# Kernel tuning notes

Hardware: AMD Instinct MI355X
Metric: run time of the kernel (lower is better)

## Reference

```python
import jax, jax.numpy as jnp
import numpy as np

B, T, D, U = 32, 4096, 256, 256


def setup_inputs() -> dict:
    key = jax.random.key(0)
    ks = jax.random.split(key, 5)
    s = 1.0 / np.sqrt(D)
    return {
        "query": jax.random.normal(ks[0], (B, D), jnp.float32),
        "values": jax.random.normal(ks[1], (B, T, D), jnp.float32),
        "W1": jax.random.normal(ks[2], (D, U), jnp.float32) * s,
        "b1": jnp.zeros((U,), jnp.float32),
        "W2": jax.random.normal(ks[3], (D, U), jnp.float32) * s,
        "b2": jnp.zeros((U,), jnp.float32),
        "V": jax.random.normal(ks[4], (U, 1), jnp.float32) * (1.0 / np.sqrt(U)),
        "bV": jnp.zeros((1,), jnp.float32),
    }


def reference(query, values, W1, b1, W2, b2, V, bV):
    # score[b,t,u] = tanh(values @ W1 + b1 + (query @ W2 + b2)[:,None,:])
    proj_v = jnp.einsum("btd,du->btu", values, W1) + b1        # [B,T,U]
    proj_q = (query @ W2 + b2)[:, None, :]                      # [B,1,U]
    score = jnp.tanh(proj_v + proj_q) @ V + bV                  # [B,T,1]
    attn = jax.nn.softmax(score, axis=1)                        # softmax over T
    context = jnp.sum(attn * values, axis=1)                    # [B,D]
    return (context, attn)
```

## Files before the change

### kernel.cpp

```cpp
#include <hip/hip_runtime.h>
#include <hip/hip_bf16.h>

typedef __attribute__((ext_vector_type(4))) float f32x4;
typedef __attribute__((ext_vector_type(8))) short s16x8;
typedef __attribute__((ext_vector_type(4))) short s16x4;

static constexpr int Bn = 32;
static constexpr int Tn = 4096;
static constexpr int Dn = 256;
static constexpr int Un = 256;
static constexpr int CH = Tn / 64;

__device__ __forceinline__ ushort f2bf(float f) {
    unsigned x = __float_as_uint(f);
    x += 0x7fffu + ((x >> 16) & 1u);
    return (ushort)(x >> 16);
}
__device__ __forceinline__ float bf2f(ushort u) {
    return __uint_as_float(((unsigned)u) << 16);
}

__device__ __forceinline__ float fast_tanh(float x) {
    float ax = fabsf(x);
    float e = __expf(-2.0f * ax);
    float r = __fdividef(1.0f - e, 1.0f + e);
    return copysignf(r, x);
}

__global__ __launch_bounds__(256) void k_prep(const float* __restrict__ W1,
                                              ushort* __restrict__ W1T,
                                              const float* __restrict__ query,
                                              const float* __restrict__ W2,
                                              const float* __restrict__ b1,
                                              const float* __restrict__ b2,
                                              float* __restrict__ qb) {
    __shared__ float qs[Dn];
    if (blockIdx.x < 256) {
        const int u = blockIdx.x, d = threadIdx.x;
        W1T[u * Dn + d] = f2bf(W1[d * Un + u]);
    } else {
        const int b = blockIdx.x - 256, u = threadIdx.x;
        qs[u] = query[b * Dn + u];
        __syncthreads();
        float acc = b1[u] + b2[u];
        #pragma unroll 8
        for (int d = 0; d < Dn; ++d) acc += qs[d] * W2[d * Un + u];
        qb[b * Un + u] = acc;
    }
}

__global__ __launch_bounds__(256, 4) void k_fused(const float* __restrict__ values,
                                                  const ushort* __restrict__ W1T,
                                                  const float* __restrict__ qb,
                                                  const float* __restrict__ Vw,
                                                  const float* __restrict__ bV,
                                                  float* __restrict__ scores,
                                                  float* __restrict__ pm,
                                                  float* __restrict__ ps,
                                                  float* __restrict__ pctx) {
    __shared__ __align__(16) ushort Al[64][264];
    __shared__ float sred[4][64];
    __shared__ float slp[64];
    __shared__ f32x4 red[4][64];
    const int tid = threadIdx.x;
    const int b = blockIdx.y;
    const int c = blockIdx.x;
    const int t0 = c * 64;
    const int wid = tid >> 6;
    const int lane = tid & 63;
    const int l15 = lane & 15;
    const int hi = lane >> 4;

    const float* vbase = values + ((size_t)b * Tn + t0) * Dn;
    #pragma unroll
    for (int i = 0; i < 8; ++i) {
        int flat = i * 2048 + tid * 8;
        int row = flat >> 8, col = flat & 255;
        const float4 f0 = *(const float4*)&vbase[row * Dn + col];
        const float4 f1 = *(const float4*)&vbase[row * Dn + col + 4];
        s16x8 p;
        p[0] = (short)f2bf(f0.x); p[1] = (short)f2bf(f0.y);
        p[2] = (short)f2bf(f0.z); p[3] = (short)f2bf(f0.w);
        p[4] = (short)f2bf(f1.x); p[5] = (short)f2bf(f1.y);
        p[6] = (short)f2bf(f1.z); p[7] = (short)f2bf(f1.w);
        *(s16x8*)&Al[row][col] = p;
    }

    const ushort* wbase = W1T + (size_t)(wid * 64 + l15) * Dn + hi * 8;

    f32x4 acc[4][4];
    #pragma unroll
    for (int tt = 0; tt < 4; ++tt)
        #pragma unroll
        for (int ut = 0; ut < 4; ++ut) acc[tt][ut] = (f32x4){0.f, 0.f, 0.f, 0.f};

    s16x8 bfn0[4], bfn1[4];
    #pragma unroll
    for (int ut = 0; ut < 4; ++ut)
        bfn0[ut] = *(const s16x8*)&wbase[(size_t)ut * 16 * Dn];
    #pragma unroll
    for (int ut = 0; ut < 4; ++ut)
        bfn1[ut] = *(const s16x8*)&wbase[(size_t)ut * 16 * Dn + 32];

    __syncthreads();

    #pragma unroll
    for (int kc = 0; kc < 8; ++kc) {
        s16x8 bf[4];
        #pragma unroll
        for (int ut = 0; ut < 4; ++ut) { bf[ut] = bfn0[ut]; bfn0[ut] = bfn1[ut]; }
        if (kc < 6) {
            #pragma unroll
            for (int ut = 0; ut < 4; ++ut)
                bfn1[ut] = *(const s16x8*)&wbase[(size_t)ut * 16 * Dn + (kc + 2) * 32];
        }
        const int k0 = kc * 32;
        s16x8 af[4];
        #pragma unroll
        for (int tt = 0; tt < 4; ++tt)
            af[tt] = *(const s16x8*)&Al[tt * 16 + l15][k0 + hi * 8];
        #pragma unroll
        for (int tt = 0; tt < 4; ++tt)
            #pragma unroll
            for (int ut = 0; ut < 4; ++ut)
                acc[tt][ut] = __builtin_amdgcn_mfma_f32_16x16x32_bf16(af[tt], bf[ut], acc[tt][ut], 0, 0, 0);
    }

    float Vreg[4], qreg[4];
    #pragma unroll
    for (int ut = 0; ut < 4; ++ut) {
        int u = wid * 64 + ut * 16 + l15;
        Vreg[ut] = Vw[u];
        qreg[ut] = qb[b * Un + u];
    }

    float psc[4][4];
    #pragma unroll
    for (int tt = 0; tt < 4; ++tt)
        #pragma unroll
        for (int i = 0; i < 4; ++i) psc[tt][i] = 0.f;
    #pragma unroll
    for (int tt = 0; tt < 4; ++tt)
        #pragma unroll
        for (int ut = 0; ut < 4; ++ut)
            #pragma unroll
            for (int i = 0; i < 4; ++i)
                psc[tt][i] += fast_tanh(acc[tt][ut][i] + qreg[ut]) * Vreg[ut];

    #pragma unroll
    for (int tt = 0; tt < 4; ++tt)
        #pragma unroll
        for (int i = 0; i < 4; ++i) {
            float v = psc[tt][i];
            v += __shfl_xor(v, 1, 64);
            v += __shfl_xor(v, 2, 64);
            v += __shfl_xor(v, 4, 64);
            v += __shfl_xor(v, 8, 64);
            if (l15 == 0) sred[wid][tt * 16 + hi * 4 + i] = v;
        }
    __syncthreads();

    if (tid < 64) {
        float s = sred[0][tid] + sred[1][tid] + sred[2][tid] + sred[3][tid] + bV[0];
        scores[b * Tn + t0 + tid] = s;
        float m = s;
        #pragma unroll
        for (int off = 32; off > 0; off >>= 1) m = fmaxf(m, __shfl_xor(m, off, 64));
        float p = __expf(s - m);
        float S = p;
        #pragma unroll
        for (int off = 32; off > 0; off >>= 1) S += __shfl_xor(S, off, 64);
        slp[tid] = p;
        if (tid == 0) { pm[b * CH + c] = m; ps[b * CH + c] = S; }
    }
    __syncthreads();

    const int d4 = (tid & 63) * 4, tg = tid >> 6;
    f32x4 a = (f32x4){0.f, 0.f, 0.f, 0.f};
    #pragma unroll 4
    for (int t = tg; t < 64; t += 4) {
        const float p = slp[t];
        const s16x4 v = *(const s16x4*)&Al[t][d4];
        a[0] += p * bf2f((ushort)v[0]);
        a[1] += p * bf2f((ushort)v[1]);
        a[2] += p * bf2f((ushort)v[2]);
        a[3] += p * bf2f((ushort)v[3]);
    }
    red[tg][tid & 63] = a;
    __syncthreads();
    if (tg == 0) {
        const f32x4 r0 = red[0][tid], r1 = red[1][tid], r2 = red[2][tid], r3 = red[3][tid];
        f32x4 o = r0 + r1 + r2 + r3;
        *(f32x4*)&pctx[((size_t)b * CH + c) * Dn + d4] = o;
    }
}

__global__ __launch_bounds__(256) void k_reduce(const float* __restrict__ pm,
                                                const float* __restrict__ ps,
                                                const float* __restrict__ pctx,
                                                float* __restrict__ context,
                                                float* __restrict__ MS) {
    const int b = blockIdx.x, d = threadIdx.x;
    float M = -1e30f;
    #pragma unroll 8
    for (int c = 0; c < CH; ++c) M = fmaxf(M, pm[b * CH + c]);
    float S = 0.f, ctx = 0.f;
    #pragma unroll 4
    for (int c = 0; c < CH; ++c) {
        const float w = __expf(pm[b * CH + c] - M);
        S += w * ps[b * CH + c];
        ctx += w * pctx[((size_t)b * CH + c) * Dn + d];
    }
    context[b * Dn + d] = __fdividef(ctx, S);
    if (d == 0) { MS[b * 2] = M; MS[b * 2 + 1] = S; }
}

__global__ __launch_bounds__(256) void k_attn(float* __restrict__ attn,
                                              const float* __restrict__ MS) {
    const int b = blockIdx.y;
    const int base = b * Tn + blockIdx.x * 1024 + threadIdx.x * 4;
    const float M = MS[b * 2];
    const float invS = __fdividef(1.0f, MS[b * 2 + 1]);
    float4 s = *(const float4*)&attn[base];
    s.x = __expf(s.x - M) * invS;
    s.y = __expf(s.y - M) * invS;
    s.z = __expf(s.z - M) * invS;
    s.w = __expf(s.w - M) * invS;
    *(float4*)&attn[base] = s;
}

extern "C" void kernel_launch(void* const* d_in, const int* in_sizes, int n_in,
                              void* d_out, int out_size, void* d_ws, size_t ws_size,
                              hipStream_t stream) {
    const float* query  = (const float*)d_in[0];
    const float* values = (const float*)d_in[1];
    const float* W1     = (const float*)d_in[2];
    const float* b1     = (const float*)d_in[3];
    const float* W2     = (const float*)d_in[4];
    const float* b2     = (const float*)d_in[5];
    const float* Vw     = (const float*)d_in[6];
    const float* bV     = (const float*)d_in[7];

    float* context = (float*)d_out;
    float* attn    = (float*)d_out + Bn * Dn;

    float*  pctx = (float*)d_ws;
    float*  pm   = pctx + (size_t)Bn * CH * Dn;
    float*  ps   = pm + Bn * CH;
    float*  qb   = ps + Bn * CH;
    float*  MS   = qb + Bn * Un;
    ushort* W1T  = (ushort*)(MS + Bn * 2);

    k_prep<<<dim3(256 + Bn), dim3(256), 0, stream>>>(W1, W1T, query, W2, b1, b2, qb);
    k_fused<<<dim3(CH, Bn), dim3(256), 0, stream>>>(values, W1T, qb, Vw, bV,
                                                    attn, pm, ps, pctx);
    k_reduce<<<dim3(Bn), dim3(256), 0, stream>>>(pm, ps, pctx, context, MS);
    k_attn<<<dim3(Tn / 1024, Bn), dim3(256), 0, stream>>>(attn, MS);
}
```

Measured before the change: 78.46 us.

## Make fused kernel persistent over 256 rows with register-staged prefetch and online softmax

Each block now loops over eight 32-row chunks of values (256 rows per block, 16 blocks per batch) instead of handling one 64-row tile. The next chunk's fp32 values are prefetched into registers while the current chunk is converted to bf16 in a double-buffered LDS tile and run through the MFMA projection. The softmax max, sum and context are accumulated online across chunks, which shrinks the partial buffers and the work in k_reduce. The cost is that W1T fragments are reloaded from global memory for every chunk, there are more barriers per chunk, and the grid drops to 512 blocks with a launch bound of 2 waves, which lowers parallelism.

```diff
diff --git a/kernel.cpp b/kernel.cpp
--- a/kernel.cpp
+++ b/kernel.cpp
@@ -9,7 +9,7 @@
 static constexpr int Tn = 4096;
 static constexpr int Dn = 256;
 static constexpr int Un = 256;
-static constexpr int CH = Tn / 64;
+static constexpr int NBLK = 16;
 
 __device__ __forceinline__ ushort f2bf(float f) {
     unsigned x = __float_as_uint(f);
@@ -49,82 +49,30 @@
     }
 }
 
-__global__ __launch_bounds__(256, 4) void k_fused(const float* __restrict__ values,
+__global__ __launch_bounds__(256, 2) void k_fused(const float* __restrict__ values,
                                                   const ushort* __restrict__ W1T,
                                                   const float* __restrict__ qb,
                                                   const float* __restrict__ Vw,
                                                   const float* __restrict__ bV,
                                                   float* __restrict__ scores,
-                                                  float* __restrict__ pm,
-                                                  float* __restrict__ ps,
+                                                  float* __restrict__ pM,
+                                                  float* __restrict__ pS,
                                                   float* __restrict__ pctx) {
-    __shared__ __align__(16) ushort Al[64][264];
-    __shared__ float sred[4][64];
-    __shared__ float slp[64];
-    __shared__ f32x4 red[4][64];
+    __shared__ __align__(16) ushort Bl[2][32][264];
+    __shared__ float sred[4][32];
+    __shared__ float slp[32];
+    __shared__ float sfac[2];
+    __shared__ float runMS[2];
+    __shared__ f32x4 cred[4][64];
+
     const int tid = threadIdx.x;
-    const int b = blockIdx.y;
-    const int c = blockIdx.x;
-    const int t0 = c * 64;
-    const int wid = tid >> 6;
-    const int lane = tid & 63;
-    const int l15 = lane & 15;
-    const int hi = lane >> 4;
-
-    const float* vbase = values + ((size_t)b * Tn + t0) * Dn;
-    #pragma unroll
-    for (int i = 0; i < 8; ++i) {
-        int flat = i * 2048 + tid * 8;
-        int row = flat >> 8, col = flat & 255;
-        const float4 f0 = *(const float4*)&vbase[row * Dn + col];
-        const float4 f1 = *(const float4*)&vbase[row * Dn + col + 4];
-        s16x8 p;
-        p[0] = (short)f2bf(f0.x); p[1] = (short)f2bf(f0.y);
-        p[2] = (short)f2bf(f0.z); p[3] = (short)f2bf(f0.w);
-        p[4] = (short)f2bf(f1.x); p[5] = (short)f2bf(f1.y);
-        p[6] = (short)f2bf(f1.z); p[7] = (short)f2bf(f1.w);
-        *(s16x8*)&Al[row][col] = p;
-    }
-
+    const int b = blockIdx.y, blk = blockIdx.x;
+    const int wid = tid >> 6, lane = tid & 63;
+    const int l15 = lane & 15, hi = lane >> 4;
+    const int d4 = (tid & 63) * 4, tg = tid >> 6;
+
+    const float* vbase = values + ((size_t)b * Tn + blk * 256) * Dn;
     const ushort* wbase = W1T + (size_t)(wid * 64 + l15) * Dn + hi * 8;
-
-    f32x4 acc[4][4];
-    #pragma unroll
-    for (int tt = 0; tt < 4; ++tt)
-        #pragma unroll
-        for (int ut = 0; ut < 4; ++ut) acc[tt][ut] = (f32x4){0.f, 0.f, 0.f, 0.f};
-
-    s16x8 bfn0[4], bfn1[4];
-    #pragma unroll
-    for (int ut = 0; ut < 4; ++ut)
-        bfn0[ut] = *(const s16x8*)&wbase[(size_t)ut * 16 * Dn];
-    #pragma unroll
-    for (int ut = 0; ut < 4; ++ut)
-        bfn1[ut] = *(const s16x8*)&wbase[(size_t)ut * 16 * Dn + 32];
-
-    __syncthreads();
-
-    #pragma unroll
-    for (int kc = 0; kc < 8; ++kc) {
-        s16x8 bf[4];
-        #pragma unroll
-        for (int ut = 0; ut < 4; ++ut) { bf[ut] = bfn0[ut]; bfn0[ut] = bfn1[ut]; }
-        if (kc < 6) {
-            #pragma unroll
-            for (int ut = 0; ut < 4; ++ut)
-                bfn1[ut] = *(const s16x8*)&wbase[(size_t)ut * 16 * Dn + (kc + 2) * 32];
-        }
-        const int k0 = kc * 32;
-        s16x8 af[4];
-        #pragma unroll
-        for (int tt = 0; tt < 4; ++tt)
-            af[tt] = *(const s16x8*)&Al[tt * 16 + l15][k0 + hi * 8];
-        #pragma unroll
-        for (int tt = 0; tt < 4; ++tt)
-            #pragma unroll
-            for (int ut = 0; ut < 4; ++ut)
-                acc[tt][ut] = __builtin_amdgcn_mfma_f32_16x16x32_bf16(af[tt], bf[ut], acc[tt][ut], 0, 0, 0);
-    }
 
     float Vreg[4], qreg[4];
     #pragma unroll
@@ -133,83 +81,167 @@
         Vreg[ut] = Vw[u];
         qreg[ut] = qb[b * Un + u];
     }
-
-    float psc[4][4];
-    #pragma unroll
-    for (int tt = 0; tt < 4; ++tt)
-        #pragma unroll
-        for (int i = 0; i < 4; ++i) psc[tt][i] = 0.f;
-    #pragma unroll
-    for (int tt = 0; tt < 4; ++tt)
+    const float bv = bV[0];
+
+    if (tid == 0) { runMS[0] = -1e30f; runMS[1] = 0.f; }
+
+    f32x4 stg[8];
+    #pragma unroll
+    for (int i = 0; i < 8; ++i) {
+        int idx = i * 256 + tid;
+        stg[i] = *(const f32x4*)&vbase[(idx >> 6) * Dn + (idx & 63) * 4];
+    }
+
+    f32x4 cacc = (f32x4){0.f, 0.f, 0.f, 0.f};
+
+    #pragma unroll 1
+    for (int ck = 0; ck < 8; ++ck) {
+        const int cur = ck & 1;
+
+        #pragma unroll
+        for (int i = 0; i < 8; ++i) {
+            int idx = i * 256 + tid;
+            s16x4 p;
+            p[0] = (short)f2bf(stg[i][0]); p[1] = (short)f2bf(stg[i][1]);
+            p[2] = (short)f2bf(stg[i][2]); p[3] = (short)f2bf(stg[i][3]);
+            *(s16x4*)&Bl[cur][idx >> 6][(idx & 63) * 4] = p;
+        }
+        __syncthreads();
+
+        if (ck < 7) {
+            const float* vb = vbase + (ck + 1) * 32 * Dn;
+            #pragma unroll
+            for (int i = 0; i < 8; ++i) {
+                int idx = i * 256 + tid;
+                stg[i] = *(const f32x4*)&vb[(idx >> 6) * Dn + (idx & 63) * 4];
+            }
+        }
+
+        s16x8 bfn0[4], bfn1[4];
         #pragma unroll
         for (int ut = 0; ut < 4; ++ut)
-            #pragma unroll
-            for (int i = 0; i < 4; ++i)
-                psc[tt][i] += fast_tanh(acc[tt][ut][i] + qreg[ut]) * Vreg[ut];
-
-    #pragma unroll
-    for (int tt = 0; tt < 4; ++tt)
-        #pragma unroll
-        for (int i = 0; i < 4; ++i) {
-            float v = psc[tt][i];
-            v += __shfl_xor(v, 1, 64);
-            v += __shfl_xor(v, 2, 64);
-            v += __shfl_xor(v, 4, 64);
-            v += __shfl_xor(v, 8, 64);
-            if (l15 == 0) sred[wid][tt * 16 + hi * 4 + i] = v;
-        }
-    __syncthreads();
-
-    if (tid < 64) {
-        float s = sred[0][tid] + sred[1][tid] + sred[2][tid] + sred[3][tid] + bV[0];
-        scores[b * Tn + t0 + tid] = s;
-        float m = s;
-        #pragma unroll
-        for (int off = 32; off > 0; off >>= 1) m = fmaxf(m, __shfl_xor(m, off, 64));
-        float p = __expf(s - m);
-        float S = p;
-        #pragma unroll
-        for (int off = 32; off > 0; off >>= 1) S += __shfl_xor(S, off, 64);
-        slp[tid] = p;
-        if (tid == 0) { pm[b * CH + c] = m; ps[b * CH + c] = S; }
-    }
-    __syncthreads();
-
-    const int d4 = (tid & 63) * 4, tg = tid >> 6;
-    f32x4 a = (f32x4){0.f, 0.f, 0.f, 0.f};
-    #pragma unroll 4
-    for (int t = tg; t < 64; t += 4) {
-        const float p = slp[t];
-        const s16x4 v = *(const s16x4*)&Al[t][d4];
-        a[0] += p * bf2f((ushort)v[0]);
-        a[1] += p * bf2f((ushort)v[1]);
-        a[2] += p * bf2f((ushort)v[2]);
-        a[3] += p * bf2f((ushort)v[3]);
-    }
-    red[tg][tid & 63] = a;
+            bfn0[ut] = *(const s16x8*)&wbase[(size_t)ut * 16 * Dn];
+        #pragma unroll
+        for (int ut = 0; ut < 4; ++ut)
+            bfn1[ut] = *(const s16x8*)&wbase[(size_t)ut * 16 * Dn + 32];
+
+        f32x4 acc[2][4];
+        #pragma unroll
+        for (int tt = 0; tt < 2; ++tt)
+            #pragma unroll
+            for (int ut = 0; ut < 4; ++ut) acc[tt][ut] = (f32x4){0.f, 0.f, 0.f, 0.f};
+
+        #pragma unroll
+        for (int kc = 0; kc < 8; ++kc) {
+            s16x8 bf[4];
+            #pragma unroll
+            for (int ut = 0; ut < 4; ++ut) { bf[ut] = bfn0[ut]; bfn0[ut] = bfn1[ut]; }
+            if (kc < 6) {
+                #pragma unroll
+                for (int ut = 0; ut < 4; ++ut)
+                    bfn1[ut] = *(const s16x8*)&wbase[(size_t)ut * 16 * Dn + (kc + 2) * 32];
+            }
+            s16x8 af[2];
+            #pragma unroll
+            for (int tt = 0; tt < 2; ++tt)
+                af[tt] = *(const s16x8*)&Bl[cur][tt * 16 + l15][kc * 32 + hi * 8];
+            #pragma unroll
+            for (int tt = 0; tt < 2; ++tt)
+                #pragma unroll
+                for (int ut = 0; ut < 4; ++ut)
+                    acc[tt][ut] = __builtin_amdgcn_mfma_f32_16x16x32_bf16(af[tt], bf[ut], acc[tt][ut], 0, 0, 0);
+        }
+
+        float psc[2][4];
+        #pragma unroll
+        for (int tt = 0; tt < 2; ++tt)
+            #pragma unroll
+            for (int i = 0; i < 4; ++i) psc[tt][i] = 0.f;
+        #pragma unroll
+        for (int tt = 0; tt < 2; ++tt)
+            #pragma unroll
+            for (int ut = 0; ut < 4; ++ut)
+                #pragma unroll
+                for (int i = 0; i < 4; ++i)
+                    psc[tt][i] += fast_tanh(acc[tt][ut][i] + qreg[ut]) * Vreg[ut];
+        #pragma unroll
+        for (int tt = 0; tt < 2; ++tt)
+            #pragma unroll
+            for (int i = 0; i < 4; ++i) {
+                float v = psc[tt][i];
+                v += __shfl_xor(v, 1, 64);
+                v += __shfl_xor(v, 2, 64);
+                v += __shfl_xor(v, 4, 64);
+                v += __shfl_xor(v, 8, 64);
+                if (l15 == 0) sred[wid][tt * 16 + hi * 4 + i] = v;
+            }
+        __syncthreads();
+
+        if (tid < 64) {
+            const int row = lane & 31;
+            float s = sred[0][row] + sred[1][row] + sred[2][row] + sred[3][row] + bv;
+            if (lane < 32) scores[b * Tn + blk * 256 + ck * 32 + row] = s;
+            float m = s;
+            #pragma unroll
+            for (int off = 16; off > 0; off >>= 1) m = fmaxf(m, __shfl_xor(m, off, 64));
+            float p = __expf(s - m);
+            float S = p;
+            #pragma unroll
+            for (int off = 16; off > 0; off >>= 1) S += __shfl_xor(S, off, 64);
+            if (lane < 32) slp[row] = p;
+            if (lane == 0) {
+                float Mold = runMS[0];
+                float Mnew = fmaxf(Mold, m);
+                float sco = __expf(Mold - Mnew);
+                float scc = __expf(m - Mnew);
+                sfac[0] = sco; sfac[1] = scc;
+                runMS[0] = Mnew;
+                runMS[1] = runMS[1] * sco + S * scc;
+            }
+        }
+        __syncthreads();
+
+        const float sco = sfac[0], scc = sfac[1];
+        f32x4 loc = (f32x4){0.f, 0.f, 0.f, 0.f};
+        #pragma unroll
+        for (int t = tg; t < 32; t += 4) {
+            const float p = slp[t];
+            const s16x4 v = *(const s16x4*)&Bl[cur][t][d4];
+            loc[0] += p * bf2f((ushort)v[0]);
+            loc[1] += p * bf2f((ushort)v[1]);
+            loc[2] += p * bf2f((ushort)v[2]);
+            loc[3] += p * bf2f((ushort)v[3]);
+        }
+        cacc = cacc * sco + loc * scc;
+    }
+
+    cred[tg][tid & 63] = cacc;
     __syncthreads();
     if (tg == 0) {
-        const f32x4 r0 = red[0][tid], r1 = red[1][tid], r2 = red[2][tid], r3 = red[3][tid];
-        f32x4 o = r0 + r1 + r2 + r3;
-        *(f32x4*)&pctx[((size_t)b * CH + c) * Dn + d4] = o;
-    }
-}
-
-__global__ __launch_bounds__(256) void k_reduce(const float* __restrict__ pm,
-                                                const float* __restrict__ ps,
+        const f32x4 o = cred[0][tid] + cred[1][tid] + cred[2][tid] + cred[3][tid];
+        *(f32x4*)&pctx[((size_t)(b * NBLK + blk)) * Dn + d4] = o;
+    }
+    if (tid == 0) {
+        pM[b * NBLK + blk] = runMS[0];
+        pS[b * NBLK + blk] = runMS[1];
+    }
+}
+
+__global__ __launch_bounds__(256) void k_reduce(const float* __restrict__ pM,
+                                                const float* __restrict__ pS,
                                                 const float* __restrict__ pctx,
                                                 float* __restrict__ context,
                                                 float* __restrict__ MS) {
     const int b = blockIdx.x, d = threadIdx.x;
     float M = -1e30f;
-    #pragma unroll 8
-    for (int c = 0; c < CH; ++c) M = fmaxf(M, pm[b * CH + c]);
+    #pragma unroll
+    for (int c = 0; c < NBLK; ++c) M = fmaxf(M, pM[b * NBLK + c]);
     float S = 0.f, ctx = 0.f;
-    #pragma unroll 4
-    for (int c = 0; c < CH; ++c) {
-        const float w = __expf(pm[b * CH + c] - M);
-        S += w * ps[b * CH + c];
-        ctx += w * pctx[((size_t)b * CH + c) * Dn + d];
+    #pragma unroll
+    for (int c = 0; c < NBLK; ++c) {
+        const float w = __expf(pM[b * NBLK + c] - M);
+        S += w * pS[b * NBLK + c];
+        ctx += w * pctx[((size_t)(b * NBLK + c)) * Dn + d];
     }
     context[b * Dn + d] = __fdividef(ctx, S);
     if (d == 0) { MS[b * 2] = M; MS[b * 2 + 1] = S; }
@@ -245,15 +277,15 @@
     float* attn    = (float*)d_out + Bn * Dn;
 
     float*  pctx = (float*)d_ws;
-    float*  pm   = pctx + (size_t)Bn * CH * Dn;
-    float*  ps   = pm + Bn * CH;
-    float*  qb   = ps + Bn * CH;
+    float*  pM   = pctx + (size_t)Bn * NBLK * Dn;
+    float*  pS   = pM + Bn * NBLK;
+    float*  qb   = pS + Bn * NBLK;
     float*  MS   = qb + Bn * Un;
     ushort* W1T  = (ushort*)(MS + Bn * 2);
 
     k_prep<<<dim3(256 + Bn), dim3(256), 0, stream>>>(W1, W1T, query, W2, b1, b2, qb);
-    k_fused<<<dim3(CH, Bn), dim3(256), 0, stream>>>(values, W1T, qb, Vw, bV,
-                                                    attn, pm, ps, pctx);
-    k_reduce<<<dim3(Bn), dim3(256), 0, stream>>>(pm, ps, pctx, context, MS);
+    k_fused<<<dim3(NBLK, Bn), dim3(256), 0, stream>>>(values, W1T, qb, Vw, bV,
+                                                      attn, pM, pS, pctx);
+    k_reduce<<<dim3(Bn), dim3(256), 0, stream>>>(pM, pS, pctx, context, MS);
     k_attn<<<dim3(Tn / 1024, Bn), dim3(256), 0, stream>>>(attn, MS);
 }
```

New measurement: 77.11 us. No clear change (-1.7%).
